# Performance work log

Hardware: AMD Instinct MI355X
Metric: run time of the kernel (lower is better)

The kernel has to match this reference:

```python
import jax, jax.numpy as jnp
import numpy as np

E, FF, H, PE = 256, 1024, 8, 32

def _ln(x, g, b, eps=1e-5):
    m = jnp.mean(x, axis=-1, keepdims=True)
    v = jnp.var(x, axis=-1, keepdims=True)
    return (x - m) / jnp.sqrt(v + eps) * g + b

def setup_inputs() -> dict:
    key = jax.random.key(0)
    ks = jax.random.split(key, 24)
    B, N, NH = 2, 8192, 8
    w = lambda i, shape: (jax.random.normal(ks[i], shape, jnp.float32) * 0.02)
    return {
        'x': jax.random.normal(ks[0], (B, N, NH, E), jnp.float32),
        'pos1': jax.random.normal(ks[1], (B, N, NH, 2), jnp.float32),
        'pos2': jax.random.normal(ks[2], (B, N, NH, 2), jnp.float32),
        'W_in': w(3, (E, E)), 'g_in': jnp.ones((E,), jnp.float32), 'b_in': jnp.zeros((E,), jnp.float32),
        'Wq': w(4, (E, E)), 'bq': jnp.zeros((E,), jnp.float32),
        'Wk': w(5, (E, E)), 'bk': jnp.zeros((E,), jnp.float32),
        'Wv': w(6, (E, E)), 'bv': jnp.zeros((E,), jnp.float32),
        'Wo': w(7, (E, E)), 'bo': jnp.zeros((E,), jnp.float32),
        'W_pos': w(8, (4, PE)), 'W_bias': w(9, (PE, H)),
        'W_ff1': w(10, (E, FF)), 'W_ff2': w(11, (FF, E)),
        'g1': jnp.ones((E,), jnp.float32), 'b1': jnp.zeros((E,), jnp.float32),
        'g2': jnp.ones((E,), jnp.float32), 'b2': jnp.zeros((E,), jnp.float32),
    }

def reference(x, pos1, pos2, W_in, g_in, b_in, Wq, bq, Wk, bk, Wv, bv, Wo, bo,
              W_pos, W_bias, W_ff1, W_ff2, g1, b1, g2, b2):
    B, N, NH, e = x.shape
    d = e // H
    # input_mlp: Linear(no bias) + LayerNorm
    t = _ln(x @ W_in, g_in, b_in).reshape(B * N, NH, e)  # (BN, nh, E); q=k=v=t
    q = (t @ Wq + bq).reshape(B * N, NH, H, d)
    k = (t @ Wk + bk).reshape(B * N, NH, H, d)
    v = (t @ Wv + bv).reshape(B * N, NH, H, d)
    scores = jnp.einsum('bqhd,bkhd->bhqk', q, k) / jnp.sqrt(jnp.float32(d))  # (BN,H,nh,nh)
    # positional bias: pos_embedder(pos1,pos2) -> emb_proj_bias -> per-key per-head bias
    emb = jax.nn.silu(jnp.concatenate([pos1, pos2], axis=-1) @ W_pos)  # (B,N,nh,PE)
    bias = (emb @ W_bias).reshape(B * N, NH, H)  # (BN, nh_key, H)
    scores = scores + jnp.transpose(bias, (0, 2, 1))[:, :, None, :]  # broadcast over queries
    att = jax.nn.softmax(scores, axis=-1)
    att_out = jnp.einsum('bhqk,bkhd->bqhd', att, v).reshape(B * N, NH, e)
    att_out = att_out @ Wo + bo
    h1 = _ln(t + att_out, g1, b1)  # q_res residual on pre-projection q
    h2 = _ln(h1 + jax.nn.silu(h1 @ W_ff1) @ W_ff2, g2, b2)
    return h2.reshape(B, N, NH, e)
```

## Files before the change

kernel.cpp:

```cpp
#include <hip/hip_runtime.h>
#include <cstdint>
#include <cstddef>

typedef unsigned short ushort_t;
typedef __attribute__((ext_vector_type(8))) short short8;
typedef __attribute__((ext_vector_type(4))) short short4v;
typedef __attribute__((ext_vector_type(4))) float floatx4;

__device__ __forceinline__ float b2f(ushort_t u) {
    unsigned v = ((unsigned)u) << 16;
    return __builtin_bit_cast(float, v);
}
__device__ __forceinline__ float b2fs(short s) { return b2f((ushort_t)s); }
__device__ __forceinline__ ushort_t f2b(float f) {
    unsigned u = __builtin_bit_cast(unsigned, f);
    u += 0x7fffu + ((u >> 16) & 1u);
    return (ushort_t)(u >> 16);
}

__device__ __forceinline__ void load_lds16(const ushort_t* g, ushort_t* l) {
    __builtin_amdgcn_global_load_lds(
        (const __attribute__((address_space(1))) void*)g,
        (__attribute__((address_space(3))) void*)l, 16, 0, 0);
}

template <int NT, bool A_F32, bool HAS_BIAS, bool DO_SILU>
__global__ __launch_bounds__(256, 2) void gemm_areg(
    const void* __restrict__ Ap, const ushort_t* __restrict__ BT,
    const float* __restrict__ bias, ushort_t* __restrict__ out)
{
    constexpr int K = 256;
    constexpr int ldN = NT * 128;
    constexpr int NH = NT * 2;
    __shared__ __align__(16) ushort_t Bs[2][64 * 256];

    const int tid = threadIdx.x;
    const int w = tid >> 6, lane = tid & 63;
    const int wm = w >> 1, wn = w & 1;
    const int quad = lane >> 4, r = lane & 15;
    const size_t m0 = (size_t)blockIdx.x * 128;

    const int srow_off = w * 2 + (lane >> 5);
    const int sslot = (lane & 31) ^ srow_off;
    const int rsw = (r & 7) << 3;

#define STAGE_H(h)                                                        \
    {                                                                     \
        const int h_ = (h);                                               \
        _Pragma("unroll")                                                 \
        for (int i_ = 0; i_ < 8; ++i_) {                                  \
            int row_ = i_ * 8 + srow_off;                                 \
            load_lds16(BT + (size_t)(h_ * 64 + row_) * K + sslot * 8,     \
                       &Bs[h_ & 1][(i_ * 8 + w * 2) * 256]);              \
        }                                                                 \
    }

    STAGE_H(0);

    short8 af[4][8];
    if (A_F32) {
        const float* A = (const float*)Ap;
#pragma unroll
        for (int mt = 0; mt < 4; ++mt) {
            const float* rp = A + (m0 + wm * 64 + mt * 16 + r) * K + quad * 8;
#pragma unroll
            for (int kk = 0; kk < 8; ++kk) {
                float4 a = *(const float4*)(rp + kk * 32);
                float4 b = *(const float4*)(rp + kk * 32 + 4);
                short8 o;
                o[0] = (short)f2b(a.x); o[1] = (short)f2b(a.y);
                o[2] = (short)f2b(a.z); o[3] = (short)f2b(a.w);
                o[4] = (short)f2b(b.x); o[5] = (short)f2b(b.y);
                o[6] = (short)f2b(b.z); o[7] = (short)f2b(b.w);
                af[mt][kk] = o;
            }
        }
    } else {
        const ushort_t* A = (const ushort_t*)Ap;
#pragma unroll
        for (int mt = 0; mt < 4; ++mt) {
            const ushort_t* rp = A + (m0 + wm * 64 + mt * 16 + r) * K + quad * 8;
#pragma unroll
            for (int kk = 0; kk < 8; ++kk)
                af[mt][kk] = *(const short8*)(rp + kk * 32);
        }
    }

    asm volatile("s_waitcnt vmcnt(0)" ::: "memory");
    __builtin_amdgcn_s_barrier();

    for (int p = 0; p < NH; ++p) {
        if (p + 1 < NH) STAGE_H(p + 1);

        floatx4 acc[2][4];
#pragma unroll
        for (int nt = 0; nt < 2; ++nt)
#pragma unroll
            for (int mt = 0; mt < 4; ++mt)
#pragma unroll
                for (int rg = 0; rg < 4; ++rg) acc[nt][mt][rg] = 0.f;

#pragma unroll
        for (int kk = 0; kk < 8; ++kk) {
            const int koff = (kk * 32 + quad * 8) ^ rsw;
#pragma unroll
            for (int nt = 0; nt < 2; ++nt) {
                int cl = wn * 32 + nt * 16 + r;
                short8 bf_ = *(const short8*)(&Bs[p & 1][cl * 256 + koff]);
#pragma unroll
                for (int mt = 0; mt < 4; ++mt)
                    acc[nt][mt] = __builtin_amdgcn_mfma_f32_16x16x32_bf16(
                        bf_, af[mt][kk], acc[nt][mt], 0, 0, 0);
            }
        }
#pragma unroll
        for (int nt = 0; nt < 2; ++nt) {
            const int colb = p * 64 + wn * 32 + nt * 16 + quad * 4;
            float b4[4] = {0.f, 0.f, 0.f, 0.f};
            if (HAS_BIAS) {
                float4 bb = *(const float4*)(bias + colb);
                b4[0] = bb.x; b4[1] = bb.y; b4[2] = bb.z; b4[3] = bb.w;
            }
#pragma unroll
            for (int mt = 0; mt < 4; ++mt) {
                size_t row = m0 + wm * 64 + mt * 16 + r;
                short4v ov;
#pragma unroll
                for (int rg = 0; rg < 4; ++rg) {
                    float v = acc[nt][mt][rg] + b4[rg];
                    if (DO_SILU) v = v / (1.f + __expf(-v));
                    ov[rg] = (short)f2b(v);
                }
                *(short4v*)(out + row * ldN + colb) = ov;
            }
        }
        asm volatile("s_waitcnt vmcnt(8)" ::: "memory");
        __builtin_amdgcn_s_barrier();
    }
#undef STAGE_H
}

__global__ __launch_bounds__(256, 2) void gemm_wide(
    const ushort_t* __restrict__ A, const ushort_t* __restrict__ BT,
    ushort_t* __restrict__ out)
{
    constexpr int K = 1024, N = 256;
    __shared__ __align__(16) ushort_t As[2][128 * 32];
    __shared__ __align__(16) ushort_t Bs[2][256 * 32];

    const int tid = threadIdx.x;
    const int w = tid >> 6, lane = tid & 63;
    const int wm = w >> 1, wn = w & 1;
    const int quad = lane >> 4, r = lane & 15;
    const size_t m0 = (size_t)blockIdx.x * 128;

    const int srow = lane >> 2;
    const int sslot = (lane & 3) ^ (srow & 3);

#define STAGE_C(c)                                                        \
    {                                                                     \
        const int c_ = (c);                                               \
        _Pragma("unroll")                                                 \
        for (int i_ = 0; i_ < 2; ++i_) {                                  \
            int rb_ = (w * 2 + i_) * 16;                                  \
            load_lds16(A + (m0 + rb_ + srow) * K + c_ * 32 + sslot * 8,   \
                       &As[c_ & 1][rb_ * 32]);                            \
        }                                                                 \
        _Pragma("unroll")                                                 \
        for (int i_ = 0; i_ < 4; ++i_) {                                  \
            int rb_ = (w * 4 + i_) * 16;                                  \
            load_lds16(BT + (size_t)(rb_ + srow) * K + c_ * 32 + sslot * 8,\
                       &Bs[c_ & 1][rb_ * 32]);                            \
        }                                                                 \
    }

    floatx4 acc[8][4];
#pragma unroll
    for (int nt = 0; nt < 8; ++nt)
#pragma unroll
        for (int mt = 0; mt < 4; ++mt)
#pragma unroll
            for (int rg = 0; rg < 4; ++rg) acc[nt][mt][rg] = 0.f;

    STAGE_C(0);
    asm volatile("s_waitcnt vmcnt(0)" ::: "memory");
    __builtin_amdgcn_s_barrier();

    const int ko = (quad ^ (r & 3)) * 8;

    for (int c = 0; c < K / 32; ++c) {
        if (c + 1 < K / 32) STAGE_C(c + 1);

        short8 af_[4];
#pragma unroll
        for (int mt = 0; mt < 4; ++mt)
            af_[mt] = *(const short8*)(&As[c & 1][(wm * 64 + mt * 16 + r) * 32 + ko]);
#pragma unroll
        for (int nt = 0; nt < 8; ++nt) {
            short8 bf_ = *(const short8*)(&Bs[c & 1][(wn * 128 + nt * 16 + r) * 32 + ko]);
#pragma unroll
            for (int mt = 0; mt < 4; ++mt)
                acc[nt][mt] = __builtin_amdgcn_mfma_f32_16x16x32_bf16(
                    bf_, af_[mt], acc[nt][mt], 0, 0, 0);
        }
        asm volatile("s_waitcnt vmcnt(0)" ::: "memory");
        __builtin_amdgcn_s_barrier();
    }
#undef STAGE_C

#pragma unroll
    for (int nt = 0; nt < 8; ++nt) {
        const int colb = wn * 128 + nt * 16 + quad * 4;
#pragma unroll
        for (int mt = 0; mt < 4; ++mt) {
            size_t row = m0 + wm * 64 + mt * 16 + r;
            short4v ov;
#pragma unroll
            for (int rg = 0; rg < 4; ++rg) ov[rg] = (short)f2b(acc[nt][mt][rg]);
            *(short4v*)(out + row * N + colb) = ov;
        }
    }
}

template <bool OUT_F32>
__global__ __launch_bounds__(256) void ln_kernel(
    const ushort_t* __restrict__ y, const ushort_t* __restrict__ res,
    const float* __restrict__ g, const float* __restrict__ b,
    void* __restrict__ outv)
{
    const int w = threadIdx.x >> 6;
    const int lane = threadIdx.x & 63;
    const size_t row = (size_t)blockIdx.x * 4 + w;
    const size_t base = row * 256 + lane * 4;

    short4v vy = *(const short4v*)(y + base);
    float v[4];
#pragma unroll
    for (int j = 0; j < 4; ++j) v[j] = b2fs(vy[j]);
    if (res) {
        short4v vr = *(const short4v*)(res + base);
#pragma unroll
        for (int j = 0; j < 4; ++j) v[j] += b2fs(vr[j]);
    }
    float s = v[0] + v[1] + v[2] + v[3];
    float sq = v[0] * v[0] + v[1] * v[1] + v[2] * v[2] + v[3] * v[3];
#pragma unroll
    for (int off = 32; off > 0; off >>= 1) {
        s += __shfl_xor(s, off, 64);
        sq += __shfl_xor(sq, off, 64);
    }
    float mean = s * (1.f / 256.f);
    float var = sq * (1.f / 256.f) - mean * mean;
    float rstd = rsqrtf(var + 1e-5f);
    if (OUT_F32) {
        float4 ov;
        int col = lane * 4;
        ov.x = (v[0] - mean) * rstd * g[col + 0] + b[col + 0];
        ov.y = (v[1] - mean) * rstd * g[col + 1] + b[col + 1];
        ov.z = (v[2] - mean) * rstd * g[col + 2] + b[col + 2];
        ov.w = (v[3] - mean) * rstd * g[col + 3] + b[col + 3];
        *(float4*)((float*)outv + base) = ov;
    } else {
        short4v ov;
#pragma unroll
        for (int j = 0; j < 4; ++j) {
            int col = lane * 4 + j;
            float o = (v[j] - mean) * rstd * g[col] + b[col];
            ov[j] = (short)f2b(o);
        }
        *(short4v*)((ushort_t*)outv + base) = ov;
    }
}

__global__ __launch_bounds__(256) void attn_kernel(
    const ushort_t* __restrict__ qkv,
    const float* __restrict__ pos1, const float* __restrict__ pos2,
    const float* __restrict__ Wpos, const float* __restrict__ Wbias,
    ushort_t* __restrict__ att_out)
{
    __shared__ __align__(16) ushort_t qkv_s[4][8 * 768];
    __shared__ float bias_s[4][8][8];
    __shared__ float wpos_s[128];
    __shared__ float wbias_s[256];

    const int tid = threadIdx.x;
    if (tid < 128) wpos_s[tid] = Wpos[tid];
    wbias_s[tid] = Wbias[tid];

    const int w = tid >> 6;
    const int lane = tid & 63;
    const int tok = blockIdx.x * 4 + w;

    const ushort_t* src = qkv + (size_t)tok * 8 * 768;
    for (int c = lane; c < 768; c += 64)
        *(short8*)(qkv_s[w] + c * 8) = *(const short8*)(src + c * 8);
    __syncthreads();

    {
        const int j = lane >> 3, h = lane & 7;
        const size_t pbase = ((size_t)tok * 8 + j) * 2;
        float p0 = pos1[pbase], p1 = pos1[pbase + 1];
        float p2 = pos2[pbase], p3 = pos2[pbase + 1];
        float acc = 0.f;
#pragma unroll
        for (int p = 0; p < 32; ++p) {
            float e = p0 * wpos_s[p] + p1 * wpos_s[32 + p] + p2 * wpos_s[64 + p] + p3 * wpos_s[96 + p];
            e = e / (1.f + __expf(-e));
            acc += e * wbias_s[p * 8 + h];
        }
        bias_s[w][j][h] = acc;
    }
    __syncthreads();

    const int i = lane >> 3, h = lane & 7;
    const ushort_t* qrow = qkv_s[w] + i * 768 + h * 32;
    float q[32];
#pragma unroll
    for (int c = 0; c < 4; ++c) {
        short8 t8 = *(const short8*)(qrow + c * 8);
#pragma unroll
        for (int e = 0; e < 8; ++e) q[c * 8 + e] = b2fs(t8[e]);
    }
    float s[8];
#pragma unroll
    for (int jj = 0; jj < 8; ++jj) {
        const ushort_t* krow = qkv_s[w] + jj * 768 + 256 + h * 32;
        float d = 0.f;
#pragma unroll
        for (int c = 0; c < 4; ++c) {
            short8 t8 = *(const short8*)(krow + c * 8);
#pragma unroll
            for (int e = 0; e < 8; ++e) d += q[c * 8 + e] * b2fs(t8[e]);
        }
        s[jj] = d * 0.17677669529663688f + bias_s[w][jj][h];
    }
    float mx = s[0];
#pragma unroll
    for (int jj = 1; jj < 8; ++jj) mx = fmaxf(mx, s[jj]);
    float l = 0.f;
#pragma unroll
    for (int jj = 0; jj < 8; ++jj) { s[jj] = __expf(s[jj] - mx); l += s[jj]; }
    float rl = 1.f / l;
    float o[32];
#pragma unroll
    for (int e = 0; e < 32; ++e) o[e] = 0.f;
#pragma unroll
    for (int jj = 0; jj < 8; ++jj) {
        float p = s[jj] * rl;
        const ushort_t* vrow = qkv_s[w] + jj * 768 + 512 + h * 32;
#pragma unroll
        for (int c = 0; c < 4; ++c) {
            short8 t8 = *(const short8*)(vrow + c * 8);
#pragma unroll
            for (int e = 0; e < 8; ++e) o[c * 8 + e] += p * b2fs(t8[e]);
        }
    }
    ushort_t* orow = att_out + ((size_t)tok * 8 + i) * 256 + h * 32;
#pragma unroll
    for (int c = 0; c < 4; ++c) {
        short8 t8;
#pragma unroll
        for (int e = 0; e < 8; ++e) t8[e] = (short)f2b(o[c * 8 + e]);
        *(short8*)(orow + c * 8) = t8;
    }
}

__global__ void transpose_kernel(const float* __restrict__ in,
                                 ushort_t* __restrict__ out, int K, int N)
{
    int idx = blockIdx.x * 256 + threadIdx.x;
    if (idx < K * N) {
        int k = idx / N, n = idx % N;
        out[n * K + k] = f2b(in[idx]);
    }
}

__global__ void pack_bias_kernel(const float* a, const float* b,
                                 const float* c, float* out)
{
    int t = blockIdx.x * 256 + threadIdx.x;
    if (t < 256) out[t] = a[t];
    else if (t < 512) out[t] = b[t - 256];
    else if (t < 768) out[t] = c[t - 512];
}

extern "C" void kernel_launch(void* const* d_in, const int* in_sizes, int n_in,
                              void* d_out, int out_size, void* d_ws, size_t ws_size,
                              hipStream_t stream)
{
    const float* x     = (const float*)d_in[0];
    const float* pos1  = (const float*)d_in[1];
    const float* pos2  = (const float*)d_in[2];
    const float* W_in  = (const float*)d_in[3];
    const float* g_in  = (const float*)d_in[4];
    const float* b_in  = (const float*)d_in[5];
    const float* Wq    = (const float*)d_in[6];
    const float* bq    = (const float*)d_in[7];
    const float* Wk    = (const float*)d_in[8];
    const float* bk    = (const float*)d_in[9];
    const float* Wv    = (const float*)d_in[10];
    const float* bv    = (const float*)d_in[11];
    const float* Wo    = (const float*)d_in[12];
    const float* bo    = (const float*)d_in[13];
    const float* W_pos = (const float*)d_in[14];
    const float* W_bias= (const float*)d_in[15];
    const float* W_ff1 = (const float*)d_in[16];
    const float* W_ff2 = (const float*)d_in[17];
    const float* g1    = (const float*)d_in[18];
    const float* b1    = (const float*)d_in[19];
    const float* g2    = (const float*)d_in[20];
    const float* b2    = (const float*)d_in[21];

    const int M = in_sizes[0] / 256;
    const int ntok = M / 8;

    ushort_t* ws    = (ushort_t*)d_ws;
    ushort_t* WinT  = ws;
    ushort_t* WqkvT = ws + 65536;
    ushort_t* WoT   = ws + 262144;
    ushort_t* Wff1T = ws + 327680;
    ushort_t* Wff2T = ws + 589824;
    float*    bqkv  = (float*)(ws + 851968);
    ushort_t* bufA  = (ushort_t*)((char*)d_ws + (2ull << 20));
    ushort_t* bufB  = bufA + (size_t)M * 256;
    ushort_t* bufC  = bufB + (size_t)M * 256;

    transpose_kernel<<<256, 256, 0, stream>>>(W_in, WinT, 256, 256);
    transpose_kernel<<<256, 256, 0, stream>>>(Wq, WqkvT, 256, 256);
    transpose_kernel<<<256, 256, 0, stream>>>(Wk, WqkvT + 65536, 256, 256);
    transpose_kernel<<<256, 256, 0, stream>>>(Wv, WqkvT + 131072, 256, 256);
    transpose_kernel<<<256, 256, 0, stream>>>(Wo, WoT, 256, 256);
    transpose_kernel<<<1024, 256, 0, stream>>>(W_ff1, Wff1T, 256, 1024);
    transpose_kernel<<<1024, 256, 0, stream>>>(W_ff2, Wff2T, 1024, 256);
    pack_bias_kernel<<<3, 256, 0, stream>>>(bq, bk, bv, bqkv);

    dim3 blk(256);
    gemm_areg<2, true, false, false><<<M / 128, blk, 0, stream>>>(x, WinT, nullptr, bufA);
    ln_kernel<false><<<M / 4, blk, 0, stream>>>(bufA, nullptr, g_in, b_in, bufB);
    gemm_areg<6, false, true, false><<<M / 128, blk, 0, stream>>>(bufB, WqkvT, bqkv, bufC);
    attn_kernel<<<ntok / 4, blk, 0, stream>>>(bufC, pos1, pos2, W_pos, W_bias, bufA);
    gemm_areg<2, false, true, false><<<M / 128, blk, 0, stream>>>(bufA, WoT, bo, bufC);
    ln_kernel<false><<<M / 4, blk, 0, stream>>>(bufC, bufB, g1, b1, bufA);
    gemm_areg<8, false, false, true><<<M / 128, blk, 0, stream>>>(bufA, Wff1T, nullptr, bufC);
    gemm_wide<<<M / 128, blk, 0, stream>>>(bufC, Wff2T, bufB);
    ln_kernel<true><<<M / 4, blk, 0, stream>>>(bufB, bufA, g2, b2, d_out);
}
```

Measured before the change: 926.8 us.

## Fuse LayerNorm epilogues into the 256-wide GEMMs and drop standalone LN kernels

Adds a gemm_ln256 kernel that keeps the full 256-column output row tile in registers and applies bias, residual and LayerNorm in the epilogue, using a small shared-memory exchange to combine row statistics across the two column warps. gemm_wide becomes gemm_wide_ln, which fuses the final residual and LayerNorm and writes fp32 output directly. This removes three separate LN launches and their bf16 round-trips through global memory. Bias loads in gemm_areg are also hoisted out of the per-head loop. In exchange the fused kernels hold more accumulator registers, which may reduce occupancy, and the Wo GEMM reads the residual from bufB while writing its output to bufB in place.

```diff
diff --git a/kernel.cpp b/kernel.cpp
--- a/kernel.cpp
+++ b/kernel.cpp
@@ -86,6 +86,16 @@
         }
     }
 
+    floatx4 bias_r[NT * 2];
+    if (HAS_BIAS) {
+#pragma unroll
+        for (int p = 0; p < NH; ++p)
+#pragma unroll
+            for (int nt = 0; nt < 2; ++nt)
+                bias_r[p * 2 + nt] =
+                    *(const floatx4*)(bias + p * 64 + wn * 32 + nt * 16 + quad * 4);
+    }
+
     asm volatile("s_waitcnt vmcnt(0)" ::: "memory");
     __builtin_amdgcn_s_barrier();
 
@@ -116,18 +126,14 @@
 #pragma unroll
         for (int nt = 0; nt < 2; ++nt) {
             const int colb = p * 64 + wn * 32 + nt * 16 + quad * 4;
-            float b4[4] = {0.f, 0.f, 0.f, 0.f};
-            if (HAS_BIAS) {
-                float4 bb = *(const float4*)(bias + colb);
-                b4[0] = bb.x; b4[1] = bb.y; b4[2] = bb.z; b4[3] = bb.w;
-            }
 #pragma unroll
             for (int mt = 0; mt < 4; ++mt) {
                 size_t row = m0 + wm * 64 + mt * 16 + r;
                 short4v ov;
 #pragma unroll
                 for (int rg = 0; rg < 4; ++rg) {
-                    float v = acc[nt][mt][rg] + b4[rg];
+                    float v = acc[nt][mt][rg];
+                    if (HAS_BIAS) v += bias_r[p * 2 + nt][rg];
                     if (DO_SILU) v = v / (1.f + __expf(-v));
                     ov[rg] = (short)f2b(v);
                 }
@@ -140,13 +146,196 @@
 #undef STAGE_H
 }
 
-__global__ __launch_bounds__(256, 2) void gemm_wide(
+template <bool A_F32, bool HAS_BIAS, bool HAS_RES, bool OUT_F32>
+__global__ __launch_bounds__(256, 2) void gemm_ln256(
+    const void* __restrict__ Ap, const ushort_t* __restrict__ BT,
+    const float* __restrict__ bias, const ushort_t* __restrict__ res,
+    const float* __restrict__ g, const float* __restrict__ b,
+    void* __restrict__ outv)
+{
+    constexpr int K = 256, NH = 4;
+    __shared__ __align__(16) ushort_t Bs[2][64 * 256];
+    __shared__ float2 redln[2][2][64];
+
+    const int tid = threadIdx.x;
+    const int w = tid >> 6, lane = tid & 63;
+    const int wm = w >> 1, wn = w & 1;
+    const int quad = lane >> 4, r = lane & 15;
+    const size_t m0 = (size_t)blockIdx.x * 128;
+
+    const int srow_off = w * 2 + (lane >> 5);
+    const int sslot = (lane & 31) ^ srow_off;
+    const int rsw = (r & 7) << 3;
+
+#define STAGE_H(h)                                                        \
+    {                                                                     \
+        const int h_ = (h);                                               \
+        _Pragma("unroll")                                                 \
+        for (int i_ = 0; i_ < 8; ++i_) {                                  \
+            int row_ = i_ * 8 + srow_off;                                 \
+            load_lds16(BT + (size_t)(h_ * 64 + row_) * K + sslot * 8,     \
+                       &Bs[h_ & 1][(i_ * 8 + w * 2) * 256]);              \
+        }                                                                 \
+    }
+
+    STAGE_H(0);
+
+    short8 af[4][8];
+    if (A_F32) {
+        const float* A = (const float*)Ap;
+#pragma unroll
+        for (int mt = 0; mt < 4; ++mt) {
+            const float* rp = A + (m0 + wm * 64 + mt * 16 + r) * K + quad * 8;
+#pragma unroll
+            for (int kk = 0; kk < 8; ++kk) {
+                float4 a = *(const float4*)(rp + kk * 32);
+                float4 bq_ = *(const float4*)(rp + kk * 32 + 4);
+                short8 o;
+                o[0] = (short)f2b(a.x); o[1] = (short)f2b(a.y);
+                o[2] = (short)f2b(a.z); o[3] = (short)f2b(a.w);
+                o[4] = (short)f2b(bq_.x); o[5] = (short)f2b(bq_.y);
+                o[6] = (short)f2b(bq_.z); o[7] = (short)f2b(bq_.w);
+                af[mt][kk] = o;
+            }
+        }
+    } else {
+        const ushort_t* A = (const ushort_t*)Ap;
+#pragma unroll
+        for (int mt = 0; mt < 4; ++mt) {
+            const ushort_t* rp = A + (m0 + wm * 64 + mt * 16 + r) * K + quad * 8;
+#pragma unroll
+            for (int kk = 0; kk < 8; ++kk)
+                af[mt][kk] = *(const short8*)(rp + kk * 32);
+        }
+    }
+
+    asm volatile("s_waitcnt vmcnt(0)" ::: "memory");
+    __builtin_amdgcn_s_barrier();
+
+    floatx4 acc[NH][2][4];
+#pragma unroll
+    for (int p = 0; p < NH; ++p)
+#pragma unroll
+        for (int nt = 0; nt < 2; ++nt)
+#pragma unroll
+            for (int mt = 0; mt < 4; ++mt)
+#pragma unroll
+                for (int rg = 0; rg < 4; ++rg) acc[p][nt][mt][rg] = 0.f;
+
+#pragma unroll
+    for (int p = 0; p < NH; ++p) {
+        if (p + 1 < NH) STAGE_H(p + 1);
+#pragma unroll
+        for (int kk = 0; kk < 8; ++kk) {
+            const int koff = (kk * 32 + quad * 8) ^ rsw;
+#pragma unroll
+            for (int nt = 0; nt < 2; ++nt) {
+                int cl = wn * 32 + nt * 16 + r;
+                short8 bf_ = *(const short8*)(&Bs[p & 1][cl * 256 + koff]);
+#pragma unroll
+                for (int mt = 0; mt < 4; ++mt)
+                    acc[p][nt][mt] = __builtin_amdgcn_mfma_f32_16x16x32_bf16(
+                        bf_, af[mt][kk], acc[p][nt][mt], 0, 0, 0);
+            }
+        }
+        if (p + 1 < NH) {
+            asm volatile("s_waitcnt vmcnt(0)" ::: "memory");
+            __builtin_amdgcn_s_barrier();
+        }
+    }
+#undef STAGE_H
+
+#pragma unroll
+    for (int p = 0; p < NH; ++p)
+#pragma unroll
+        for (int nt = 0; nt < 2; ++nt) {
+            const int colb = p * 64 + wn * 32 + nt * 16 + quad * 4;
+            floatx4 bv;
+            if (HAS_BIAS) bv = *(const floatx4*)(bias + colb);
+#pragma unroll
+            for (int mt = 0; mt < 4; ++mt) {
+                if (HAS_BIAS)
+#pragma unroll
+                    for (int rg = 0; rg < 4; ++rg) acc[p][nt][mt][rg] += bv[rg];
+                if (HAS_RES) {
+                    size_t row = m0 + wm * 64 + mt * 16 + r;
+                    short4v rv = *(const short4v*)(res + row * 256 + colb);
+#pragma unroll
+                    for (int rg = 0; rg < 4; ++rg)
+                        acc[p][nt][mt][rg] += b2fs(rv[rg]);
+                }
+            }
+        }
+
+    float s[4], sq[4];
+#pragma unroll
+    for (int mt = 0; mt < 4; ++mt) {
+        float ts = 0.f, tq = 0.f;
+#pragma unroll
+        for (int p = 0; p < NH; ++p)
+#pragma unroll
+            for (int nt = 0; nt < 2; ++nt)
+#pragma unroll
+                for (int rg = 0; rg < 4; ++rg) {
+                    float v = acc[p][nt][mt][rg];
+                    ts += v; tq += v * v;
+                }
+        ts += __shfl_xor(ts, 16, 64); ts += __shfl_xor(ts, 32, 64);
+        tq += __shfl_xor(tq, 16, 64); tq += __shfl_xor(tq, 32, 64);
+        s[mt] = ts; sq[mt] = tq;
+    }
+    if (quad == 0) {
+#pragma unroll
+        for (int mt = 0; mt < 4; ++mt)
+            redln[wm][wn][mt * 16 + r] = make_float2(s[mt], sq[mt]);
+    }
+    __syncthreads();
+    float mean[4], rstd[4];
+#pragma unroll
+    for (int mt = 0; mt < 4; ++mt) {
+        float2 o = redln[wm][wn ^ 1][mt * 16 + r];
+        float stot = s[mt] + o.x, sqtot = sq[mt] + o.y;
+        mean[mt] = stot * (1.f / 256.f);
+        float var = sqtot * (1.f / 256.f) - mean[mt] * mean[mt];
+        rstd[mt] = rsqrtf(var + 1e-5f);
+    }
+
+#pragma unroll
+    for (int p = 0; p < NH; ++p)
+#pragma unroll
+        for (int nt = 0; nt < 2; ++nt) {
+            const int colb = p * 64 + wn * 32 + nt * 16 + quad * 4;
+            floatx4 gg = *(const floatx4*)(g + colb);
+            floatx4 bb = *(const floatx4*)(b + colb);
+#pragma unroll
+            for (int mt = 0; mt < 4; ++mt) {
+                size_t row = m0 + wm * 64 + mt * 16 + r;
+                if (OUT_F32) {
+                    floatx4 ov;
+#pragma unroll
+                    for (int rg = 0; rg < 4; ++rg)
+                        ov[rg] = (acc[p][nt][mt][rg] - mean[mt]) * rstd[mt] * gg[rg] + bb[rg];
+                    *(floatx4*)((float*)outv + row * 256 + colb) = ov;
+                } else {
+                    short4v ov;
+#pragma unroll
+                    for (int rg = 0; rg < 4; ++rg)
+                        ov[rg] = (short)f2b((acc[p][nt][mt][rg] - mean[mt]) * rstd[mt] * gg[rg] + bb[rg]);
+                    *(short4v*)((ushort_t*)outv + row * 256 + colb) = ov;
+                }
+            }
+        }
+}
+
+__global__ __launch_bounds__(256, 2) void gemm_wide_ln(
     const ushort_t* __restrict__ A, const ushort_t* __restrict__ BT,
-    ushort_t* __restrict__ out)
+    const ushort_t* __restrict__ res, const float* __restrict__ g,
+    const float* __restrict__ b, float* __restrict__ out)
 {
     constexpr int K = 1024, N = 256;
     __shared__ __align__(16) ushort_t As[2][128 * 32];
     __shared__ __align__(16) ushort_t Bs[2][256 * 32];
+    __shared__ float2 redln[2][2][64];
 
     const int tid = threadIdx.x;
     const int w = tid >> 6, lane = tid & 63;
@@ -214,61 +403,57 @@
 #pragma unroll
         for (int mt = 0; mt < 4; ++mt) {
             size_t row = m0 + wm * 64 + mt * 16 + r;
-            short4v ov;
-#pragma unroll
-            for (int rg = 0; rg < 4; ++rg) ov[rg] = (short)f2b(acc[nt][mt][rg]);
-            *(short4v*)(out + row * N + colb) = ov;
-        }
-    }
-}
-
-template <bool OUT_F32>
-__global__ __launch_bounds__(256) void ln_kernel(
-    const ushort_t* __restrict__ y, const ushort_t* __restrict__ res,
-    const float* __restrict__ g, const float* __restrict__ b,
-    void* __restrict__ outv)
-{
-    const int w = threadIdx.x >> 6;
-    const int lane = threadIdx.x & 63;
-    const size_t row = (size_t)blockIdx.x * 4 + w;
-    const size_t base = row * 256 + lane * 4;
-
-    short4v vy = *(const short4v*)(y + base);
-    float v[4];
-#pragma unroll
-    for (int j = 0; j < 4; ++j) v[j] = b2fs(vy[j]);
-    if (res) {
-        short4v vr = *(const short4v*)(res + base);
-#pragma unroll
-        for (int j = 0; j < 4; ++j) v[j] += b2fs(vr[j]);
-    }
-    float s = v[0] + v[1] + v[2] + v[3];
-    float sq = v[0] * v[0] + v[1] * v[1] + v[2] * v[2] + v[3] * v[3];
-#pragma unroll
-    for (int off = 32; off > 0; off >>= 1) {
-        s += __shfl_xor(s, off, 64);
-        sq += __shfl_xor(sq, off, 64);
-    }
-    float mean = s * (1.f / 256.f);
-    float var = sq * (1.f / 256.f) - mean * mean;
-    float rstd = rsqrtf(var + 1e-5f);
-    if (OUT_F32) {
-        float4 ov;
-        int col = lane * 4;
-        ov.x = (v[0] - mean) * rstd * g[col + 0] + b[col + 0];
-        ov.y = (v[1] - mean) * rstd * g[col + 1] + b[col + 1];
-        ov.z = (v[2] - mean) * rstd * g[col + 2] + b[col + 2];
-        ov.w = (v[3] - mean) * rstd * g[col + 3] + b[col + 3];
-        *(float4*)((float*)outv + base) = ov;
-    } else {
-        short4v ov;
-#pragma unroll
-        for (int j = 0; j < 4; ++j) {
-            int col = lane * 4 + j;
-            float o = (v[j] - mean) * rstd * g[col] + b[col];
-            ov[j] = (short)f2b(o);
-        }
-        *(short4v*)((ushort_t*)outv + base) = ov;
+            short4v rv = *(const short4v*)(res + row * 256 + colb);
+#pragma unroll
+            for (int rg = 0; rg < 4; ++rg) acc[nt][mt][rg] += b2fs(rv[rg]);
+        }
+    }
+
+    float s[4], sq[4];
+#pragma unroll
+    for (int mt = 0; mt < 4; ++mt) {
+        float ts = 0.f, tq = 0.f;
+#pragma unroll
+        for (int nt = 0; nt < 8; ++nt)
+#pragma unroll
+            for (int rg = 0; rg < 4; ++rg) {
+                float v = acc[nt][mt][rg];
+                ts += v; tq += v * v;
+            }
+        ts += __shfl_xor(ts, 16, 64); ts += __shfl_xor(ts, 32, 64);
+        tq += __shfl_xor(tq, 16, 64); tq += __shfl_xor(tq, 32, 64);
+        s[mt] = ts; sq[mt] = tq;
+    }
+    if (quad == 0) {
+#pragma unroll
+        for (int mt = 0; mt < 4; ++mt)
+            redln[wm][wn][mt * 16 + r] = make_float2(s[mt], sq[mt]);
+    }
+    __syncthreads();
+    float mean[4], rstd[4];
+#pragma unroll
+    for (int mt = 0; mt < 4; ++mt) {
+        float2 o = redln[wm][wn ^ 1][mt * 16 + r];
+        float stot = s[mt] + o.x, sqtot = sq[mt] + o.y;
+        mean[mt] = stot * (1.f / 256.f);
+        float var = sqtot * (1.f / 256.f) - mean[mt] * mean[mt];
+        rstd[mt] = rsqrtf(var + 1e-5f);
+    }
+
+#pragma unroll
+    for (int nt = 0; nt < 8; ++nt) {
+        const int colb = wn * 128 + nt * 16 + quad * 4;
+        floatx4 gg = *(const floatx4*)(g + colb);
+        floatx4 bb = *(const floatx4*)(b + colb);
+#pragma unroll
+        for (int mt = 0; mt < 4; ++mt) {
+            size_t row = m0 + wm * 64 + mt * 16 + r;
+            floatx4 ov;
+#pragma unroll
+            for (int rg = 0; rg < 4; ++rg)
+                ov[rg] = (acc[nt][mt][rg] - mean[mt]) * rstd[mt] * gg[rg] + bb[rg];
+            *(floatx4*)(out + row * 256 + colb) = ov;
+        }
     }
 }
 
@@ -435,13 +620,12 @@
     pack_bias_kernel<<<3, 256, 0, stream>>>(bq, bk, bv, bqkv);
 
     dim3 blk(256);
-    gemm_areg<2, true, false, false><<<M / 128, blk, 0, stream>>>(x, WinT, nullptr, bufA);
-    ln_kernel<false><<<M / 4, blk, 0, stream>>>(bufA, nullptr, g_in, b_in, bufB);
+    gemm_ln256<true, false, false, false><<<M / 128, blk, 0, stream>>>(
+        x, WinT, nullptr, nullptr, g_in, b_in, bufB);
     gemm_areg<6, false, true, false><<<M / 128, blk, 0, stream>>>(bufB, WqkvT, bqkv, bufC);
     attn_kernel<<<ntok / 4, blk, 0, stream>>>(bufC, pos1, pos2, W_pos, W_bias, bufA);
-    gemm_areg<2, false, true, false><<<M / 128, blk, 0, stream>>>(bufA, WoT, bo, bufC);
-    ln_kernel<false><<<M / 4, blk, 0, stream>>>(bufC, bufB, g1, b1, bufA);
-    gemm_areg<8, false, false, true><<<M / 128, blk, 0, stream>>>(bufA, Wff1T, nullptr, bufC);
-    gemm_wide<<<M / 128, blk, 0, stream>>>(bufC, Wff2T, bufB);
-    ln_kernel<true><<<M / 4, blk, 0, stream>>>(bufB, bufA, g2, b2, d_out);
-}
+    gemm_ln256<false, true, true, false><<<M / 128, blk, 0, stream>>>(
+        bufA, WoT, bo, bufB, g1, b1, bufB);
+    gemm_areg<8, false, false, true><<<M / 128, blk, 0, stream>>>(bufB, Wff1T, nullptr, bufC);
+    gemm_wide_ln<<<M / 128, blk, 0, stream>>>(bufC, Wff2T, bufB, g2, b2, (float*)d_out);
+}
```

Measured after the change: 976.5 us. 5.4% more time.

## Fuse final LayerNorm and residual into FF2 GEMM epilogue; use fast reciprocal

Applied to the files above, without the earlier changes.

Folds the residual add and the final LayerNorm into the epilogue of the FF2 GEMM. Row statistics are reduced across the two column-warps through shared memory, and the output is written directly as fp32. This removes one kernel launch and a bf16 round trip of the intermediate tensor. Separately, biases are preloaded into registers before the GEMM loop, and SiLU and softmax normalisation switch to the approximate rcp instruction, which slightly lowers precision and raises register pressure.

```diff
diff --git a/kernel.cpp b/kernel.cpp
--- a/kernel.cpp
+++ b/kernel.cpp
@@ -16,6 +16,9 @@
     unsigned u = __builtin_bit_cast(unsigned, f);
     u += 0x7fffu + ((u >> 16) & 1u);
     return (ushort_t)(u >> 16);
+}
+__device__ __forceinline__ float fast_silu(float v) {
+    return v * __builtin_amdgcn_rcpf(1.f + __expf(-v));
 }
 
 __device__ __forceinline__ void load_lds16(const ushort_t* g, ushort_t* l) {
@@ -86,6 +89,16 @@
         }
     }
 
+    floatx4 bias_r[NT * 4];
+    if (HAS_BIAS) {
+#pragma unroll
+        for (int p = 0; p < NH; ++p)
+#pragma unroll
+            for (int nt = 0; nt < 2; ++nt)
+                bias_r[p * 2 + nt] =
+                    *(const floatx4*)(bias + p * 64 + wn * 32 + nt * 16 + quad * 4);
+    }
+
     asm volatile("s_waitcnt vmcnt(0)" ::: "memory");
     __builtin_amdgcn_s_barrier();
 
@@ -116,19 +129,15 @@
 #pragma unroll
         for (int nt = 0; nt < 2; ++nt) {
             const int colb = p * 64 + wn * 32 + nt * 16 + quad * 4;
-            float b4[4] = {0.f, 0.f, 0.f, 0.f};
-            if (HAS_BIAS) {
-                float4 bb = *(const float4*)(bias + colb);
-                b4[0] = bb.x; b4[1] = bb.y; b4[2] = bb.z; b4[3] = bb.w;
-            }
 #pragma unroll
             for (int mt = 0; mt < 4; ++mt) {
                 size_t row = m0 + wm * 64 + mt * 16 + r;
                 short4v ov;
 #pragma unroll
                 for (int rg = 0; rg < 4; ++rg) {
-                    float v = acc[nt][mt][rg] + b4[rg];
-                    if (DO_SILU) v = v / (1.f + __expf(-v));
+                    float v = acc[nt][mt][rg];
+                    if (HAS_BIAS) v += bias_r[p * 2 + nt][rg];
+                    if (DO_SILU) v = fast_silu(v);
                     ov[rg] = (short)f2b(v);
                 }
                 *(short4v*)(out + row * ldN + colb) = ov;
@@ -140,13 +149,15 @@
 #undef STAGE_H
 }
 
-__global__ __launch_bounds__(256, 2) void gemm_wide(
+__global__ __launch_bounds__(256, 2) void gemm_wide_ln(
     const ushort_t* __restrict__ A, const ushort_t* __restrict__ BT,
-    ushort_t* __restrict__ out)
+    const ushort_t* __restrict__ res, const float* __restrict__ g,
+    const float* __restrict__ b, float* __restrict__ out)
 {
     constexpr int K = 1024, N = 256;
     __shared__ __align__(16) ushort_t As[2][128 * 32];
     __shared__ __align__(16) ushort_t Bs[2][256 * 32];
+    __shared__ float2 redln[2][2][64];
 
     const int tid = threadIdx.x;
     const int w = tid >> 6, lane = tid & 63;
@@ -214,10 +225,56 @@
 #pragma unroll
         for (int mt = 0; mt < 4; ++mt) {
             size_t row = m0 + wm * 64 + mt * 16 + r;
-            short4v ov;
-#pragma unroll
-            for (int rg = 0; rg < 4; ++rg) ov[rg] = (short)f2b(acc[nt][mt][rg]);
-            *(short4v*)(out + row * N + colb) = ov;
+            short4v rv = *(const short4v*)(res + row * 256 + colb);
+#pragma unroll
+            for (int rg = 0; rg < 4; ++rg) acc[nt][mt][rg] += b2fs(rv[rg]);
+        }
+    }
+
+    float s[4], sq[4];
+#pragma unroll
+    for (int mt = 0; mt < 4; ++mt) {
+        float ts = 0.f, tq = 0.f;
+#pragma unroll
+        for (int nt = 0; nt < 8; ++nt)
+#pragma unroll
+            for (int rg = 0; rg < 4; ++rg) {
+                float v = acc[nt][mt][rg];
+                ts += v; tq += v * v;
+            }
+        ts += __shfl_xor(ts, 16, 64); ts += __shfl_xor(ts, 32, 64);
+        tq += __shfl_xor(tq, 16, 64); tq += __shfl_xor(tq, 32, 64);
+        s[mt] = ts; sq[mt] = tq;
+    }
+    if (quad == 0) {
+#pragma unroll
+        for (int mt = 0; mt < 4; ++mt)
+            redln[wm][wn][mt * 16 + r] = make_float2(s[mt], sq[mt]);
+    }
+    __syncthreads();
+    float mean[4], rstd[4];
+#pragma unroll
+    for (int mt = 0; mt < 4; ++mt) {
+        float2 o = redln[wm][wn ^ 1][mt * 16 + r];
+        float stot = s[mt] + o.x, sqtot = sq[mt] + o.y;
+        mean[mt] = stot * (1.f / 256.f);
+        float var = sqtot * (1.f / 256.f) - mean[mt] * mean[mt];
+        rstd[mt] = rsqrtf(var + 1e-5f);
+    }
+
+#pragma unroll
+    for (int nt = 0; nt < 8; ++nt) {
+        const int colb = wn * 128 + nt * 16 + quad * 4;
+        floatx4 gg = *(const floatx4*)(g + colb);
+        floatx4 bb = *(const floatx4*)(b + colb);
+#pragma unroll
+        for (int mt = 0; mt < 4; ++mt) {
+            size_t row = m0 + wm * 64 + mt * 16 + r;
+            floatx4 ov;
+#pragma unroll
+            for (int rg = 0; rg < 4; ++rg)
+                ov[rg] = (acc[nt][mt][rg] - mean[mt]) * rstd[mt] * gg[rg] + bb[rg];
+            *(floatx4*)(out + row * 256 + colb) = ov;
         }
     }
 }
@@ -305,7 +362,7 @@
 #pragma unroll
         for (int p = 0; p < 32; ++p) {
             float e = p0 * wpos_s[p] + p1 * wpos_s[32 + p] + p2 * wpos_s[64 + p] + p3 * wpos_s[96 + p];
-            e = e / (1.f + __expf(-e));
+            e = fast_silu(e);
             acc += e * wbias_s[p * 8 + h];
         }
         bias_s[w][j][h] = acc;
@@ -340,7 +397,7 @@
     float l = 0.f;
 #pragma unroll
     for (int jj = 0; jj < 8; ++jj) { s[jj] = __expf(s[jj] - mx); l += s[jj]; }
-    float rl = 1.f / l;
+    float rl = __builtin_amdgcn_rcpf(l);
     float o[32];
 #pragma unroll
     for (int e = 0; e < 32; ++e) o[e] = 0.f;
@@ -442,6 +499,5 @@
     gemm_areg<2, false, true, false><<<M / 128, blk, 0, stream>>>(bufA, WoT, bo, bufC);
     ln_kernel<false><<<M / 4, blk, 0, stream>>>(bufC, bufB, g1, b1, bufA);
     gemm_areg<8, false, false, true><<<M / 128, blk, 0, stream>>>(bufA, Wff1T, nullptr, bufC);
-    gemm_wide<<<M / 128, blk, 0, stream>>>(bufC, Wff2T, bufB);
-    ln_kernel<true><<<M / 4, blk, 0, stream>>>(bufB, bufA, g2, b2, d_out);
-}
+    gemm_wide_ln<<<M / 128, blk, 0, stream>>>(bufC, Wff2T, bufA, g2, b2, (float*)d_out);
+}
```

Result: no change. 939.8 us (+1.4%).
